# Kernel tuning notes

Hardware: AMD Instinct MI355X
Metric: run time of the kernel (lower is better)

Reference implementation:

```python
import jax, jax.numpy as jnp
import numpy as np

LEAKY_SLOPE = 0.01  # torch F.leaky_relu default


def _l2norm(x):
    # matches F.normalize(p=2, dim=-1, eps=1e-12)
    n = jnp.linalg.norm(x, axis=-1, keepdims=True)
    return x / jnp.maximum(n, 1e-12)


def setup_inputs() -> dict:
    key = jax.random.key(0)
    k1, k2, k3, k4 = jax.random.split(key, 4)
    B, S, H = 16, 256, 768
    return {
        "query_embs": jax.random.normal(k1, (B, S, H), dtype=jnp.float32),
        "key_embs": jax.random.normal(k2, (2 * B, S, H), dtype=jnp.float32),
        "logit_scale": jnp.log(jnp.asarray(1.0 / 0.07, dtype=jnp.float32)),
        "alpha_raw": jnp.asarray(1.0, dtype=jnp.float32),
        "q_mask": jax.random.randint(k3, (B, S), 0, 2).astype(jnp.int32),
        "k_mask": jax.random.randint(k4, (2 * B, S), 0, 2).astype(jnp.int32),
    }


def reference(query_embs, key_embs, logit_scale, alpha_raw, q_mask, k_mask):
    q = _l2norm(query_embs)                 # [B, S, H]
    k = _l2norm(key_embs)                   # [2B, S, H]
    S = q.shape[1]

    # all-pairs token similarity: [B, 2B, S, S]
    sim = jnp.einsum('ish,jth->ijst', q, k)

    # exponential distance weighting
    pos = jnp.arange(S)
    dist = jnp.abs(pos[:, None] - pos[None, :]).astype(sim.dtype)
    alpha = jax.nn.leaky_relu(alpha_raw, LEAKY_SLOPE)
    sim = sim * jnp.exp(-alpha * dist)

    # joint validity mask: q_mask[i,s] & k_mask[j,t]
    valid = (q_mask[:, None, :, None] * k_mask[None, :, None, :]) > 0

    logits = jnp.where(valid, jnp.exp(logit_scale) * sim, -jnp.inf)
    p = jnp.nan_to_num(jax.nn.softmax(logits, axis=-1), nan=0.0)  # fully-masked rows -> 0

    # softmax-weighted aggregation of key tokens, then dot with query tokens
    agg = jnp.einsum('ijst,jth->ijsh', p, k)        # [B, 2B, S, H]
    per_tok = jnp.einsum('ish,ijsh->ijs', q, agg)   # [B, 2B, S]
    per_tok = per_tok * q_mask[:, None, :].astype(per_tok.dtype)
    return per_tok.sum(axis=-1)                     # [B, 2B]
```

## Files before the change

kernel.cpp:

```cpp
#include <hip/hip_runtime.h>
#include <hip/hip_bf16.h>

#define BQ   16
#define BK2  32
#define SEQ  256
#define HD   768

typedef __attribute__((ext_vector_type(8))) short bf16x8;
typedef __attribute__((ext_vector_type(4))) float f32x4;

__device__ __forceinline__ void glds16(const unsigned short* g, unsigned short* l) {
    __builtin_amdgcn_global_load_lds(
        (const __attribute__((address_space(1))) unsigned int*)g,
        (__attribute__((address_space(3))) unsigned int*)l, 16, 0, 0);
}

__device__ inline unsigned short f2bf(float x) {
    __hip_bfloat16 h = __float2bfloat16(x);
    union { __hip_bfloat16 h; unsigned short u; } c; c.h = h;
    return c.u;
}

__global__ __launch_bounds__(256) void norm_kernel(
    const float* __restrict__ q, const float* __restrict__ k,
    unsigned short* __restrict__ qn, unsigned short* __restrict__ kn)
{
    int row  = blockIdx.x * 4 + (threadIdx.x >> 6);
    int lane = threadIdx.x & 63;
    const int NQ = BQ * SEQ;
    const float* src = (row < NQ) ? q + (size_t)row * HD
                                  : k + (size_t)(row - NQ) * HD;
    unsigned short* dst = (row < NQ) ? qn + (size_t)row * HD
                                     : kn + (size_t)(row - NQ) * HD;
    float4 v[3];
    float ss = 0.f;
#pragma unroll
    for (int c = 0; c < 3; ++c) {
        v[c] = ((const float4*)src)[lane + 64 * c];
        ss += v[c].x * v[c].x + v[c].y * v[c].y + v[c].z * v[c].z + v[c].w * v[c].w;
    }
#pragma unroll
    for (int m = 1; m < 64; m <<= 1) ss += __shfl_xor(ss, m, 64);
    float inv = 1.f / fmaxf(sqrtf(ss), 1e-12f);
#pragma unroll
    for (int c = 0; c < 3; ++c) {
        ushort4 o = make_ushort4(f2bf(v[c].x * inv), f2bf(v[c].y * inv),
                                 f2bf(v[c].z * inv), f2bf(v[c].w * inv));
        ((ushort4*)dst)[lane + 64 * c] = o;
    }
}

__global__ __launch_bounds__(256, 3) void li_kernel(
    const unsigned short* __restrict__ qn, const unsigned short* __restrict__ kn,
    const float* __restrict__ g_ls, const float* __restrict__ g_ar,
    const int* __restrict__ k_mask, float2* __restrict__ pw)
{
    const int j  = blockIdx.x, i = blockIdx.y;
    const int sh = blockIdx.z >> 1, th = blockIdx.z & 1;
    const int tid  = threadIdx.x;
    const int w    = tid >> 6, lane = tid & 63;
    const int ln   = lane & 15, lg = lane >> 4;
    const int wsd  = w >> 1, wt = w & 1;

    __shared__ __align__(16) unsigned short As[128 * 64];
    __shared__ __align__(16) unsigned short Bs[128 * 64];
    __shared__ float w2[SEQ];
    __shared__ float kmB[128];

    float a0 = g_ar[0];
    float alpha = (a0 > 0.f) ? a0 : 0.01f * a0;
    float scale = __expf(g_ls[0]);
    w2[tid] = scale * __expf(-alpha * (float)tid);
    if (tid < 128) kmB[tid] = (k_mask[j * SEQ + th * 128 + tid] != 0) ? 1.f : 0.f;

    const int rl  = lane >> 3;
    const int gch = (lane & 7) ^ rl;
    const unsigned short* aq = qn + ((size_t)i * SEQ + sh * 128 + w * 8 + rl) * HD + gch * 8;
    const unsigned short* bq = kn + ((size_t)j * SEQ + th * 128 + w * 8 + rl) * HD + gch * 8;
    unsigned short* al = As + (w * 8) * 64;
    unsigned short* bl = Bs + (w * 8) * 64;

    f32x4 acc[4][4];
    const f32x4 zero4 = {0.f, 0.f, 0.f, 0.f};
#pragma unroll
    for (int a = 0; a < 4; ++a)
#pragma unroll
        for (int b = 0; b < 4; ++b) acc[a][b] = zero4;

    for (int kk = 0; kk < HD; kk += 64) {
        __syncthreads();
#pragma unroll
        for (int c = 0; c < 4; ++c) {
            glds16(aq + kk + c * (32 * HD), al + c * (32 * 64));
            glds16(bq + kk + c * (32 * HD), bl + c * (32 * 64));
        }
        __syncthreads();
        const bf16x8* A8 = (const bf16x8*)As;
        const bf16x8* B8 = (const bf16x8*)Bs;
#pragma unroll
        for (int ks = 0; ks < 2; ++ks) {
            const int ch = (ks * 4 + lg) ^ (ln & 7);
            bf16x8 af[4], bfr[4];
#pragma unroll
            for (int rm = 0; rm < 4; ++rm)
                af[rm] = A8[(wsd * 64 + rm * 16 + ln) * 8 + ch];
#pragma unroll
            for (int cn = 0; cn < 4; ++cn)
                bfr[cn] = B8[(wt * 64 + cn * 16 + ln) * 8 + ch];
#pragma unroll
            for (int rm = 0; rm < 4; ++rm)
#pragma unroll
                for (int cn = 0; cn < 4; ++cn)
                    acc[rm][cn] = __builtin_amdgcn_mfma_f32_16x16x32_bf16(
                        af[rm], bfr[cn], acc[rm][cn], 0, 0, 0);
        }
    }

    float kmv[4];
#pragma unroll
    for (int cn = 0; cn < 4; ++cn) kmv[cn] = kmB[wt * 64 + cn * 16 + ln];
    const int tg = th * 128 + wt * 64 + ln;

#pragma unroll
    for (int rm = 0; rm < 4; ++rm)
#pragma unroll
        for (int r = 0; r < 4; ++r) {
            int sl = wsd * 64 + rm * 16 + lg * 4 + r;
            int s  = sh * 128 + sl;
            float ze = 0.f, we = 0.f;
#pragma unroll
            for (int cn = 0; cn < 4; ++cn) {
                int t = tg + cn * 16;
                float sim = acc[rm][cn][r];
                int d = s - t; d = (d < 0) ? -d : d;
                float e = kmv[cn] * __expf(sim * w2[d]);
                ze += e;
                we = fmaf(e, sim, we);
            }
#pragma unroll
            for (int m = 1; m < 16; m <<= 1) {
                ze += __shfl_xor(ze, m, 64);
                we += __shfl_xor(we, m, 64);
            }
            if (ln == 0) {
                size_t idx = ((size_t)((i * BK2 + j) * SEQ) + s) * 4 + th * 2 + wt;
                pw[idx] = make_float2(ze, we);
            }
        }
}

__global__ __launch_bounds__(256) void reduce_kernel(
    const float2* __restrict__ pw, const int* __restrict__ q_mask,
    float* __restrict__ out)
{
    int j = blockIdx.x, i = blockIdx.y, s = threadIdx.x;
    const float4* p = (const float4*)(pw + ((size_t)(i * BK2 + j) * SEQ + s) * 4);
    float4 a = p[0], b = p[1];
    float Z = a.x + a.z + b.x + b.z;
    float W = a.y + a.w + b.y + b.w;
    float pt = (Z > 0.f) ? (W / Z) : 0.f;
    pt *= (float)q_mask[i * SEQ + s];
#pragma unroll
    for (int m = 1; m < 64; m <<= 1) pt += __shfl_xor(pt, m, 64);
    __shared__ float rb[4];
    int wv = s >> 6, lane = s & 63;
    if (lane == 0) rb[wv] = pt;
    __syncthreads();
    if (s == 0) out[i * BK2 + j] = rb[0] + rb[1] + rb[2] + rb[3];
}

extern "C" void kernel_launch(void* const* d_in, const int* in_sizes, int n_in,
                              void* d_out, int out_size, void* d_ws, size_t ws_size,
                              hipStream_t stream) {
    const float* q  = (const float*)d_in[0];
    const float* k  = (const float*)d_in[1];
    const float* ls = (const float*)d_in[2];
    const float* ar = (const float*)d_in[3];
    const int* qm   = (const int*)d_in[4];
    const int* km   = (const int*)d_in[5];
    float* out      = (float*)d_out;

    unsigned short* qn = (unsigned short*)d_ws;
    unsigned short* kn = qn + (size_t)BQ * SEQ * HD;
    float2* pw = (float2*)((char*)d_ws + (size_t)(BQ + BK2) * SEQ * HD * 2);

    norm_kernel<<<(BQ + BK2) * SEQ / 4, 256, 0, stream>>>(q, k, qn, kn);
    li_kernel<<<dim3(BK2, BQ, 4), 256, 0, stream>>>(qn, kn, ls, ar, km, pw);
    reduce_kernel<<<dim3(BK2, BQ), 256, 0, stream>>>(pw, qm, out);
}
```

Baseline: 149.7 us.

## Fuse reduction into similarity kernel with 128x256 tiles and atomic accumulation

The similarity kernel now runs 512-thread blocks that cover the full 256-token key axis for each 128-query half. Row sums are finished in shared memory and each block atomically adds its partial to the output, which removes the separate reduce kernel and its global partials buffer. The norm kernel zeroes the output, uses rsqrt, and packs bf16 pairs with manual rounding. This saves one launch and global traffic and reuses each A tile across twice as many key columns. In exchange the grid has half as many blocks, occupancy per block is lower, and float atomics make the summation order nondeterministic.

Result: faster. 141.1 us (-5.8%).

```diff
diff --git a/kernel.cpp b/kernel.cpp
--- a/kernel.cpp
+++ b/kernel.cpp
@@ -15,23 +15,28 @@
         (__attribute__((address_space(3))) unsigned int*)l, 16, 0, 0);
 }
 
-__device__ inline unsigned short f2bf(float x) {
-    __hip_bfloat16 h = __float2bfloat16(x);
-    union { __hip_bfloat16 h; unsigned short u; } c; c.h = h;
-    return c.u;
+__device__ __forceinline__ unsigned int pack2_bf16(float a, float b) {
+    unsigned ua = __float_as_uint(a), ub = __float_as_uint(b);
+    ua += 0x7FFFu + ((ua >> 16) & 1u);
+    ub += 0x7FFFu + ((ub >> 16) & 1u);
+    return (ua >> 16) | (ub & 0xFFFF0000u);
 }
 
 __global__ __launch_bounds__(256) void norm_kernel(
     const float* __restrict__ q, const float* __restrict__ k,
-    unsigned short* __restrict__ qn, unsigned short* __restrict__ kn)
+    unsigned short* __restrict__ qn, unsigned short* __restrict__ kn,
+    float* __restrict__ out)
 {
+    if (blockIdx.x == 0 && threadIdx.x < 256) {
+        out[threadIdx.x] = 0.f; out[threadIdx.x + 256] = 0.f;
+    }
     int row  = blockIdx.x * 4 + (threadIdx.x >> 6);
     int lane = threadIdx.x & 63;
     const int NQ = BQ * SEQ;
     const float* src = (row < NQ) ? q + (size_t)row * HD
                                   : k + (size_t)(row - NQ) * HD;
-    unsigned short* dst = (row < NQ) ? qn + (size_t)row * HD
-                                     : kn + (size_t)(row - NQ) * HD;
+    unsigned int* dst = (unsigned int*)((row < NQ) ? qn + (size_t)row * HD
+                                                   : kn + (size_t)(row - NQ) * HD);
     float4 v[3];
     float ss = 0.f;
 #pragma unroll
@@ -41,42 +46,43 @@
     }
 #pragma unroll
     for (int m = 1; m < 64; m <<= 1) ss += __shfl_xor(ss, m, 64);
-    float inv = 1.f / fmaxf(sqrtf(ss), 1e-12f);
+    float inv = rsqrtf(fmaxf(ss, 1e-24f));
 #pragma unroll
     for (int c = 0; c < 3; ++c) {
-        ushort4 o = make_ushort4(f2bf(v[c].x * inv), f2bf(v[c].y * inv),
-                                 f2bf(v[c].z * inv), f2bf(v[c].w * inv));
-        ((ushort4*)dst)[lane + 64 * c] = o;
+        uint2 o = make_uint2(pack2_bf16(v[c].x * inv, v[c].y * inv),
+                             pack2_bf16(v[c].z * inv, v[c].w * inv));
+        ((uint2*)dst)[lane + 64 * c] = o;
     }
 }
 
-__global__ __launch_bounds__(256, 3) void li_kernel(
+__global__ __launch_bounds__(512, 2) void li_kernel(
     const unsigned short* __restrict__ qn, const unsigned short* __restrict__ kn,
     const float* __restrict__ g_ls, const float* __restrict__ g_ar,
-    const int* __restrict__ k_mask, float2* __restrict__ pw)
+    const int* __restrict__ q_mask, const int* __restrict__ k_mask,
+    float* __restrict__ out)
 {
-    const int j  = blockIdx.x, i = blockIdx.y;
-    const int sh = blockIdx.z >> 1, th = blockIdx.z & 1;
+    const int j  = blockIdx.x, i = blockIdx.y, sh = blockIdx.z;
     const int tid  = threadIdx.x;
     const int w    = tid >> 6, lane = tid & 63;
     const int ln   = lane & 15, lg = lane >> 4;
-    const int wsd  = w >> 1, wt = w & 1;
+    const int wsd  = w >> 2, wt = w & 3;
 
     __shared__ __align__(16) unsigned short As[128 * 64];
-    __shared__ __align__(16) unsigned short Bs[128 * 64];
+    __shared__ __align__(16) unsigned short Bs[256 * 64];
     __shared__ float w2[SEQ];
-    __shared__ float kmB[128];
+    __shared__ float kmB[SEQ];
+    __shared__ float red[8];
 
     float a0 = g_ar[0];
     float alpha = (a0 > 0.f) ? a0 : 0.01f * a0;
     float scale = __expf(g_ls[0]);
-    w2[tid] = scale * __expf(-alpha * (float)tid);
-    if (tid < 128) kmB[tid] = (k_mask[j * SEQ + th * 128 + tid] != 0) ? 1.f : 0.f;
+    if (tid < 256) w2[tid] = scale * __expf(-alpha * (float)tid);
+    else           kmB[tid - 256] = (k_mask[j * SEQ + (tid - 256)] != 0) ? 1.f : 0.f;
 
     const int rl  = lane >> 3;
     const int gch = (lane & 7) ^ rl;
     const unsigned short* aq = qn + ((size_t)i * SEQ + sh * 128 + w * 8 + rl) * HD + gch * 8;
-    const unsigned short* bq = kn + ((size_t)j * SEQ + th * 128 + w * 8 + rl) * HD + gch * 8;
+    const unsigned short* bq = kn + ((size_t)j * SEQ + w * 8 + rl) * HD + gch * 8;
     unsigned short* al = As + (w * 8) * 64;
     unsigned short* bl = Bs + (w * 8) * 64;
 
@@ -89,11 +95,11 @@
 
     for (int kk = 0; kk < HD; kk += 64) {
         __syncthreads();
+        glds16(aq + kk,           al);
+        glds16(aq + kk + 64 * HD, al + 64 * 64);
 #pragma unroll
-        for (int c = 0; c < 4; ++c) {
-            glds16(aq + kk + c * (32 * HD), al + c * (32 * 64));
-            glds16(bq + kk + c * (32 * HD), bl + c * (32 * 64));
-        }
+        for (int c = 0; c < 4; ++c)
+            glds16(bq + kk + c * (64 * HD), bl + c * (64 * 64));
         __syncthreads();
         const bf16x8* A8 = (const bf16x8*)As;
         const bf16x8* B8 = (const bf16x8*)Bs;
@@ -116,24 +122,23 @@
         }
     }
 
-    float kmv[4];
-#pragma unroll
-    for (int cn = 0; cn < 4; ++cn) kmv[cn] = kmB[wt * 64 + cn * 16 + ln];
-    const int tg = th * 128 + wt * 64 + ln;
+    __syncthreads();
+    float* zs  = (float*)As;
+    float* wsc = zs + 512;
 
 #pragma unroll
     for (int rm = 0; rm < 4; ++rm)
 #pragma unroll
         for (int r = 0; r < 4; ++r) {
-            int sl = wsd * 64 + rm * 16 + lg * 4 + r;
-            int s  = sh * 128 + sl;
+            int srow = wsd * 64 + rm * 16 + lg * 4 + r;
+            int s  = sh * 128 + srow;
             float ze = 0.f, we = 0.f;
 #pragma unroll
             for (int cn = 0; cn < 4; ++cn) {
-                int t = tg + cn * 16;
+                int t = wt * 64 + cn * 16 + ln;
                 float sim = acc[rm][cn][r];
                 int d = s - t; d = (d < 0) ? -d : d;
-                float e = kmv[cn] * __expf(sim * w2[d]);
+                float e = kmB[t] * __expf(sim * w2[d]);
                 ze += e;
                 we = fmaf(e, sim, we);
             }
@@ -142,31 +147,28 @@
                 ze += __shfl_xor(ze, m, 64);
                 we += __shfl_xor(we, m, 64);
             }
-            if (ln == 0) {
-                size_t idx = ((size_t)((i * BK2 + j) * SEQ) + s) * 4 + th * 2 + wt;
-                pw[idx] = make_float2(ze, we);
-            }
+            if (ln == 0) { zs[srow * 4 + wt] = ze; wsc[srow * 4 + wt] = we; }
         }
-}
+    __syncthreads();
 
-__global__ __launch_bounds__(256) void reduce_kernel(
-    const float2* __restrict__ pw, const int* __restrict__ q_mask,
-    float* __restrict__ out)
-{
-    int j = blockIdx.x, i = blockIdx.y, s = threadIdx.x;
-    const float4* p = (const float4*)(pw + ((size_t)(i * BK2 + j) * SEQ + s) * 4);
-    float4 a = p[0], b = p[1];
-    float Z = a.x + a.z + b.x + b.z;
-    float W = a.y + a.w + b.y + b.w;
-    float pt = (Z > 0.f) ? (W / Z) : 0.f;
-    pt *= (float)q_mask[i * SEQ + s];
+    float part = 0.f;
+    if (tid < 128) {
+        const float4 Z4 = ((const float4*)zs)[tid];
+        const float4 W4 = ((const float4*)wsc)[tid];
+        float Z = Z4.x + Z4.y + Z4.z + Z4.w;
+        float W = W4.x + W4.y + W4.z + W4.w;
+        float pt = (Z > 0.f) ? (W / Z) : 0.f;
+        part = pt * (float)q_mask[i * SEQ + sh * 128 + tid];
+    }
 #pragma unroll
-    for (int m = 1; m < 64; m <<= 1) pt += __shfl_xor(pt, m, 64);
-    __shared__ float rb[4];
-    int wv = s >> 6, lane = s & 63;
-    if (lane == 0) rb[wv] = pt;
+    for (int m = 1; m < 64; m <<= 1) part += __shfl_xor(part, m, 64);
+    if (lane == 0) red[w] = part;
     __syncthreads();
-    if (s == 0) out[i * BK2 + j] = rb[0] + rb[1] + rb[2] + rb[3];
+    if (tid == 0) {
+        float tot = red[0] + red[1] + red[2] + red[3]
+                  + red[4] + red[5] + red[6] + red[7];
+        atomicAdd(&out[i * BK2 + j], tot);
+    }
 }
 
 extern "C" void kernel_launch(void* const* d_in, const int* in_sizes, int n_in,
@@ -182,9 +184,7 @@
 
     unsigned short* qn = (unsigned short*)d_ws;
     unsigned short* kn = qn + (size_t)BQ * SEQ * HD;
-    float2* pw = (float2*)((char*)d_ws + (size_t)(BQ + BK2) * SEQ * HD * 2);
 
-    norm_kernel<<<(BQ + BK2) * SEQ / 4, 256, 0, stream>>>(q, k, qn, kn);
-    li_kernel<<<dim3(BK2, BQ, 4), 256, 0, stream>>>(qn, kn, ls, ar, km, pw);
-    reduce_kernel<<<dim3(BK2, BQ), 256, 0, stream>>>(pw, qm, out);
+    norm_kernel<<<(BQ + BK2) * SEQ / 4, 256, 0, stream>>>(q, k, qn, kn, (float*)d_out);
+    li_kernel<<<dim3(BK2, BQ, 2), 512, 0, stream>>>(qn, kn, ls, ar, qm, km, (float*)d_out);
 }
```
